# Performance work log

Hardware: AMD Instinct MI355X
Metric: run time of the kernel (lower is better)

Reference implementation:

```python
import jax, jax.numpy as jnp
import numpy as np

B, C, H, W, HEADS = 4, 192, 128, 128, 8
C2 = 2 * C
DN = ('NCHW', 'OIHW', 'NCHW')


def conv1x1(x, w, b):
    o = jax.lax.conv_general_dilated(x, w, (1, 1), 'VALID', dimension_numbers=DN)
    return o + b[None, :, None, None]


def gconv3(x, w, b):
    # grouped 3x3 conv: groups = C, channels = 2C -> 2 in / 2 out channels per group
    o = jax.lax.conv_general_dilated(x, w, (1, 1), 'SAME', dimension_numbers=DN,
                                     feature_group_count=C)
    return o + b[None, :, None, None]


def l2norm(t):
    # torch F.normalize(dim=-1, eps=1e-12)
    n = jnp.linalg.norm(t, axis=-1, keepdims=True)
    return t / jnp.maximum(n, 1e-12)


def setup_inputs() -> dict:
    key = jax.random.key(0)
    ks = jax.random.split(key, 16)
    s = 0.02
    inp = {
        'x': jax.random.normal(ks[0], (B, C, H, W), jnp.float32),
        'y': jax.random.normal(ks[1], (B, C, H, W), jnp.float32),
        'kv_w': jax.random.normal(ks[2], (C2, C, 1, 1), jnp.float32) * s,
        'kv_b': jax.random.normal(ks[3], (C2,), jnp.float32) * s,
        'kv_dw_w': jax.random.normal(ks[4], (C2, 2, 3, 3), jnp.float32) * s,
        'kv_dw_b': jax.random.normal(ks[5], (C2,), jnp.float32) * s,
        'q_w': jax.random.normal(ks[6], (C2, C, 1, 1), jnp.float32) * s,
        'q_b': jax.random.normal(ks[7], (C2,), jnp.float32) * s,
        'q_dw_w': jax.random.normal(ks[8], (C2, 2, 3, 3), jnp.float32) * s,
        'q_dw_b': jax.random.normal(ks[9], (C2,), jnp.float32) * s,
        'ky_w': jax.random.normal(ks[10], (C2, C, 1, 1), jnp.float32) * s,
        'ky_b': jax.random.normal(ks[11], (C2,), jnp.float32) * s,
        'ky_dw_w': jax.random.normal(ks[12], (C2, 2, 3, 3), jnp.float32) * s,
        'ky_dw_b': jax.random.normal(ks[13], (C2,), jnp.float32) * s,
        'temperature': jnp.ones((HEADS, 1, 1), jnp.float32),
        'gamma1': jnp.full((1,), 0.1, jnp.float32),
        'gamma2': jnp.full((1,), 0.1, jnp.float32),
    }
    return inp


def reference(x, y, kv_w, kv_b, kv_dw_w, kv_dw_b, q_w, q_b, q_dw_w, q_dw_b,
              ky_w, ky_b, ky_dw_w, ky_dw_b, temperature, gamma1, gamma2):
    b, c, h, w = x.shape
    ch = c // HEADS  # channels per head

    x_mid = x + y
    q = gconv3(conv1x1(x_mid, kv_w, kv_b), kv_dw_w, kv_dw_b)
    q1, q2 = jnp.split(q, 2, axis=1)
    kvx = gconv3(conv1x1(x, q_w, q_b), q_dw_w, q_dw_b)
    kx, vx = jnp.split(kvx, 2, axis=1)
    kvy = gconv3(conv1x1(y, ky_w, ky_b), ky_dw_w, ky_dw_b)
    ky_, vy = jnp.split(kvy, 2, axis=1)

    def to_heads(t):  # (b, head*ch, h, w) -> (b, head, ch, h*w)
        return t.reshape(b, HEADS, ch, h * w)

    q1, q2, kx, ky_, vx, vy = map(to_heads, (q1, q2, kx, ky_, vx, vy))
    q1, q2, kx, ky_ = map(l2norm, (q1, q2, kx, ky_))

    attn = (jnp.einsum('bhcn,bhdn->bhcd', q1, ky_) +
            jnp.einsum('bhcn,bhdn->bhcd', q2, kx)) * temperature[None]
    attn = jax.nn.softmax(attn, axis=-1)  # (b, head, c, c), tiny c

    out1 = jnp.einsum('bhcd,bhdn->bhcn', attn, vx)
    out2 = jnp.einsum('bhcd,bhdn->bhcn', attn, vy)
    out = gamma1[0] * out1 + gamma2[0] * out2
    return out.reshape(b, c, h, w)
```

## Files before the change

kernel.cpp:

```cpp
#include <hip/hip_runtime.h>
#include <hip/hip_bf16.h>
#include <stdint.h>

#define NUM_B 4
#define NUM_C 192
#define NUM_C2 384
#define NUM_H 128
#define NUM_W 128
#define NUM_N 16384
#define NHEADS 8
#define CHD 24

#define NKC 128
#define PSTRIDE 1280
#define LROWF 132

typedef float f32x4_t __attribute__((ext_vector_type(4)));
typedef float f32x2_t __attribute__((ext_vector_type(2)));
typedef __bf16 bf16x8_t __attribute__((ext_vector_type(8)));
typedef unsigned short u16x8_t __attribute__((ext_vector_type(8)));
typedef unsigned short u16x4_t __attribute__((ext_vector_type(4)));

__device__ __forceinline__ float bf2f(unsigned short u){
  union { unsigned int i; float f; } v; v.i = ((unsigned int)u) << 16; return v.f;
}
__device__ __forceinline__ unsigned short f2bf(float f){
  union { float f; unsigned int i; } v; v.f = f;
  unsigned int x = v.i;
  x += 0x7fffu + ((x >> 16) & 1u);
  return (unsigned short)(x >> 16);
}
__device__ __forceinline__ unsigned short f2bf_n(float f){
  union { __bf16 h; unsigned short u; } cv; cv.h = (__bf16)f; return cv.u;
}

__global__ __launch_bounds__(256) void prepack_w3(
    const float* __restrict__ W0, const float* __restrict__ W1,
    const float* __restrict__ W2, unsigned short* __restrict__ out)
{
  int tid = blockIdx.x * 256 + threadIdx.x;
  if (tid >= 9216) return;
  const float* W = (blockIdx.y == 0) ? W0 : (blockIdx.y == 1) ? W1 : W2;
  unsigned short* o_ = out + (size_t)blockIdx.y * 73728;
  int c = tid & 3;
  int o = (tid >> 2) & 127;
  int s = (tid >> 9) % 6;
  int ot = tid / 3072;
  int sw = c ^ ((o >> 1) & 3);
  const float* src = W + (size_t)(ot * 128 + o) * NUM_C + s * 32 + sw * 8;
  f32x4_t f0 = *(const f32x4_t*)src;
  f32x4_t f1 = *(const f32x4_t*)(src + 4);
  u16x8_t pk;
  pk[0] = f2bf(f0[0]); pk[1] = f2bf(f0[1]); pk[2] = f2bf(f0[2]); pk[3] = f2bf(f0[3]);
  pk[4] = f2bf(f1[0]); pk[5] = f2bf(f1[1]); pk[6] = f2bf(f1[2]); pk[7] = f2bf(f1[3]);
  *(u16x8_t*)(o_ + (size_t)tid * 8) = pk;
}

__global__ __launch_bounds__(256) void prepack_in(
    const float* __restrict__ x, const float* __restrict__ y,
    unsigned short* __restrict__ xb, unsigned short* __restrict__ yb)
{
  __shared__ __align__(16) float LX[32 * LROWF];
  __shared__ __align__(16) float LY[32 * LROWF];
  const int t = threadIdx.x;
  const int nt = blockIdx.x, s = blockIdx.y, b = blockIdx.z;
  const float* px = x + (size_t)b * NUM_C * NUM_N + (size_t)s * 32 * NUM_N + nt * 128;
  const float* py = y + (size_t)b * NUM_C * NUM_N + (size_t)s * 32 * NUM_N + nt * 128;
  #pragma unroll
  for (int i = 0; i < 4; i++){
    int idx = t + 256 * i;
    int k = idx >> 5, n4 = idx & 31;
    f32x4_t vx4 = *(const f32x4_t*)(px + (size_t)k * NUM_N + n4 * 4);
    f32x4_t vy4 = *(const f32x4_t*)(py + (size_t)k * NUM_N + n4 * 4);
    int col = (n4 * 4) ^ ((k >> 3) << 3);
    *(f32x4_t*)(&LX[k * LROWF + col]) = vx4;
    *(f32x4_t*)(&LY[k * LROWF + col]) = vy4;
  }
  __syncthreads();
  size_t obase = ((size_t)(b * 128 + nt) * 6 + s) * 4096;
  #pragma unroll
  for (int i = 0; i < 2; i++){
    int u = t + 256 * i;
    int n = u >> 2, slot = u & 3;
    int c = slot ^ ((n >> 1) & 3);
    int colr = n ^ (c << 3);
    u16x8_t ox, oy;
    #pragma unroll
    for (int kk = 0; kk < 8; kk++){
      ox[kk] = f2bf_n(LX[(c * 8 + kk) * LROWF + colr]);
      oy[kk] = f2bf_n(LY[(c * 8 + kk) * LROWF + colr]);
    }
    *(u16x8_t*)(xb + obase + (size_t)u * 8) = ox;
    *(u16x8_t*)(yb + obase + (size_t)u * 8) = oy;
  }
}

__global__ __launch_bounds__(256, 4) void conv1x1_fused(
    const unsigned short* __restrict__ xb, const unsigned short* __restrict__ yb,
    const unsigned short* __restrict__ Wpk,
    const float* __restrict__ b0, const float* __restrict__ b1,
    const float* __restrict__ b2, unsigned short* __restrict__ z3)
{
  __shared__ __align__(16) unsigned short As[2][4096];
  __shared__ __align__(16) unsigned short Bs[2][4096];
  const int d = blockIdx.x;
  const int xcd = d & 7;
  const int rest = d >> 3;
  const int j = rest % 9;
  const int m_ = (rest / 9) * 8 + xcd;
  const int br = j / 3;
  const int ot = j % 3;
  const int nt = m_ & 127;
  const int b  = m_ >> 7;
  const int t = threadIdx.x;
  const int lane = t & 63;
  const int wv = t >> 6;
  const int wr = wv >> 1, wc = wv & 1;
  const int n0 = nt * 128;

  const unsigned short* Bp0 = (br == 2) ? yb : xb;
  const unsigned short* Bp1 = yb;
  const int add2 = (br == 0);
  const unsigned short* Wb = Wpk + (size_t)br * 73728;
  const float* bias = (br == 0) ? b0 : (br == 1) ? b1 : b2;
  unsigned short* zout = z3 + (size_t)br * NUM_B * NUM_C2 * NUM_N;

  f32x4_t acc[4][4];
  const f32x4_t zz = {0.f, 0.f, 0.f, 0.f};
  #pragma unroll
  for (int m = 0; m < 4; m++)
    #pragma unroll
    for (int nf = 0; nf < 4; nf++) acc[m][nf] = zz;

  u16x8_t areg[2], breg[2], breg2[2];

  auto loadA = [&](int ks){
    const u16x8_t* gp = (const u16x8_t*)(Wb + (size_t)(ot * 6 + ks) * 4096);
    areg[0] = gp[t];
    areg[1] = gp[t + 256];
  };
  auto loadB = [&](int ks){
    size_t off = ((size_t)(b * 128 + nt) * 6 + ks) * 4096;
    const u16x8_t* gp = (const u16x8_t*)(Bp0 + off);
    breg[0] = gp[t];
    breg[1] = gp[t + 256];
    if (add2){
      const u16x8_t* gp2 = (const u16x8_t*)(Bp1 + off);
      breg2[0] = gp2[t];
      breg2[1] = gp2[t + 256];
    }
  };
  auto writeA = [&](int buf){
    *(u16x8_t*)(&As[buf][(size_t)t * 8]) = areg[0];
    *(u16x8_t*)(&As[buf][(size_t)(t + 256) * 8]) = areg[1];
  };
  auto writeB = [&](int buf){
    if (!add2){
      *(u16x8_t*)(&Bs[buf][(size_t)t * 8]) = breg[0];
      *(u16x8_t*)(&Bs[buf][(size_t)(t + 256) * 8]) = breg[1];
    } else {
      #pragma unroll
      for (int i = 0; i < 2; i++){
        u16x8_t r;
        #pragma unroll
        for (int jj = 0; jj < 8; jj++)
          r[jj] = f2bf_n(bf2f(breg[i][jj]) + bf2f(breg2[i][jj]));
        *(u16x8_t*)(&Bs[buf][(size_t)(t + 256 * i) * 8]) = r;
      }
    }
  };

  auto compute = [&](int buf){
    const int rsel = lane & 15;
    const int g = lane >> 4;
    bf16x8_t af[4], bfr[4];
    #pragma unroll
    for (int m = 0; m < 4; m++){
      int r = wr * 64 + m * 16 + rsel;
      int sw = g ^ ((r >> 1) & 3);
      af[m] = *(const bf16x8_t*)(&As[buf][r * 32 + sw * 8]);
    }
    #pragma unroll
    for (int nf = 0; nf < 4; nf++){
      int r = wc * 64 + nf * 16 + rsel;
      int sw = g ^ ((r >> 1) & 3);
      bfr[nf] = *(const bf16x8_t*)(&Bs[buf][r * 32 + sw * 8]);
    }
    #pragma unroll
    for (int m = 0; m < 4; m++)
      #pragma unroll
      for (int nf = 0; nf < 4; nf++)
        acc[m][nf] = __builtin_amdgcn_mfma_f32_16x16x32_bf16(af[m], bfr[nf], acc[m][nf], 0, 0, 0);
  };

  loadA(0); loadB(0);
  writeA(0); writeB(0);
  __syncthreads();
  int buf = 0;
  #pragma unroll 1
  for (int ks = 0; ks < 6; ks++){
    if (ks < 5){
      loadA(ks + 1);
      loadB(ks + 1);
    }
    compute(buf);
    if (ks < 5){
      writeA(buf ^ 1);
      writeB(buf ^ 1);
      __syncthreads();
    }
    buf ^= 1;
  }

  const int colb = lane & 15;
  const int ob_l = lane >> 4;
  #pragma unroll
  for (int m = 0; m < 4; m++){
    int o_blk = ot * 32 + wr * 16 + m * 4 + ob_l;
    #pragma unroll
    for (int nf = 0; nf < 4; nf++){
      int col = n0 + wc * 64 + nf * 16 + colb;
      u16x4_t pk;
      #pragma unroll
      for (int r = 0; r < 4; r++)
        pk[r] = f2bf_n(acc[m][nf][r] + bias[o_blk * 4 + r]);
      *(u16x4_t*)(zout + (((size_t)b * 96 + o_blk) * NUM_N + col) * 4) = pk;
    }
  }
}

__global__ __launch_bounds__(256) void gconv4_dw(
    const unsigned short* __restrict__ zp,
    const float* __restrict__ dww, const float* __restrict__ dwb,
    unsigned short* __restrict__ outq)
{
  const int t = threadIdx.x;
  const int wo = t & 15;
  const int hh = t >> 4;
  const int h = blockIdx.x * 16 + hh;
  const int g2 = blockIdx.y;
  const int b = blockIdx.z;

  float v[4][3][8];
  const unsigned short* src = zp + (size_t)(b * 96 + g2) * NUM_N * 4;
  #pragma unroll
  for (int dy = 0; dy < 3; dy++){
    int row = h + dy - 1;
    if (row >= 0 && row < NUM_H){
      const unsigned short* base = src + (size_t)(row * NUM_W + wo * 8) * 4;
      u16x8_t ch[4];
      #pragma unroll
      for (int q = 0; q < 4; q++) ch[q] = *(const u16x8_t*)(base + q * 8);
      #pragma unroll
      for (int jw = 0; jw < 8; jw++)
        #pragma unroll
        for (int c = 0; c < 4; c++){
          int idx = jw * 4 + c;
          v[c][dy][jw] = bf2f(ch[idx >> 3][idx & 7]);
        }
    } else {
      #pragma unroll
      for (int c = 0; c < 4; c++)
        #pragma unroll
        for (int jw = 0; jw < 8; jw++) v[c][dy][jw] = 0.f;
    }
  }
  float lft[4][3], rgt[4][3];
  #pragma unroll
  for (int c = 0; c < 4; c++)
    #pragma unroll
    for (int dy = 0; dy < 3; dy++){
      float l = __shfl_up(v[c][dy][7], 1u, 64);
      float r = __shfl_down(v[c][dy][0], 1u, 64);
      lft[c][dy] = (wo == 0)  ? 0.f : l;
      rgt[c][dy] = (wo == 15) ? 0.f : r;
    }
  #pragma unroll
  for (int c = 0; c < 4; c++){
    const int oc = g2 * 4 + c;
    const int ci0 = c & 2;
    float wgt[2][9];
    #pragma unroll
    for (int icg = 0; icg < 2; icg++)
      #pragma unroll
      for (int k9 = 0; k9 < 9; k9++)
        wgt[icg][k9] = dww[(size_t)oc * 18 + icg * 9 + k9];
    float bia = dwb[oc];
    u16x8_t st;
    #pragma unroll
    for (int w8 = 0; w8 < 8; w8++){
      float s = bia;
      #pragma unroll
      for (int icg = 0; icg < 2; icg++){
        const int ci = ci0 + icg;
        #pragma unroll
        for (int ky = 0; ky < 3; ky++)
          #pragma unroll
          for (int kx = 0; kx < 3; kx++){
            int wx = w8 + kx - 1;
            float xv = (wx < 0) ? lft[ci][ky] : ((wx > 7) ? rgt[ci][ky] : v[ci][ky][wx]);
            s += wgt[icg][ky * 3 + kx] * xv;
          }
      }
      st[w8] = f2bf(s);
    }
    *(u16x8_t*)(outq + ((size_t)b * NUM_C2 + oc) * NUM_N + h * NUM_W + wo * 8) = st;
  }
}

__global__ __launch_bounds__(64) void dots_kernel(
    const unsigned short* __restrict__ qkv0, const unsigned short* __restrict__ qkv1,
    const unsigned short* __restrict__ qkv2, float* __restrict__ dpart)
{
  const int lane = threadIdx.x;
  const int kc = blockIdx.x;
  const int h = blockIdx.y;
  const int b = blockIdx.z;
  const unsigned short* q1 = qkv0 + ((size_t)b * NUM_C2 + h * CHD) * NUM_N;
  const unsigned short* q2 = qkv0 + ((size_t)b * NUM_C2 + NUM_C + h * CHD) * NUM_N;
  const unsigned short* kx = qkv1 + ((size_t)b * NUM_C2 + h * CHD) * NUM_N;
  const unsigned short* ky = qkv2 + ((size_t)b * NUM_C2 + h * CHD) * NUM_N;

  const f32x4_t zz = {0.f, 0.f, 0.f, 0.f};
  f32x4_t d1[2][2], d2[2][2], nrm[4][2];
  #pragma unroll
  for (int i = 0; i < 2; i++)
    #pragma unroll
    for (int j = 0; j < 2; j++){ d1[i][j] = zz; d2[i][j] = zz; }
  #pragma unroll
  for (int tn = 0; tn < 4; tn++){ nrm[tn][0] = zz; nrm[tn][1] = zz; }

  const int row = lane & 15;
  const int kl = (lane >> 4) * 8;
  const int r0 = row;
  const int r1 = (16 + row < CHD) ? (16 + row) : (CHD - 1);
  #pragma unroll
  for (int ks = 0; ks < 4; ks++){
    const size_t k0 = (size_t)kc * 128 + ks * 32 + kl;
    const size_t off0 = (size_t)r0 * NUM_N + k0;
    const size_t off1 = (size_t)r1 * NUM_N + k0;
    bf16x8_t fq1[2], fq2[2], fkx[2], fky[2];
    fq1[0] = *(const bf16x8_t*)(q1 + off0);  fq1[1] = *(const bf16x8_t*)(q1 + off1);
    fq2[0] = *(const bf16x8_t*)(q2 + off0);  fq2[1] = *(const bf16x8_t*)(q2 + off1);
    fkx[0] = *(const bf16x8_t*)(kx + off0);  fkx[1] = *(const bf16x8_t*)(kx + off1);
    fky[0] = *(const bf16x8_t*)(ky + off0);  fky[1] = *(const bf16x8_t*)(ky + off1);
    #pragma unroll
    for (int i = 0; i < 2; i++)
      #pragma unroll
      for (int j = 0; j < 2; j++){
        d1[i][j] = __builtin_amdgcn_mfma_f32_16x16x32_bf16(fq1[i], fky[j], d1[i][j], 0, 0, 0);
        d2[i][j] = __builtin_amdgcn_mfma_f32_16x16x32_bf16(fq2[i], fkx[j], d2[i][j], 0, 0, 0);
      }
    #pragma unroll
    for (int rg = 0; rg < 2; rg++){
      nrm[0][rg] = __builtin_amdgcn_mfma_f32_16x16x32_bf16(fq1[rg], fq1[rg], nrm[0][rg], 0, 0, 0);
      nrm[1][rg] = __builtin_amdgcn_mfma_f32_16x16x32_bf16(fq2[rg], fq2[rg], nrm[1][rg], 0, 0, 0);
      nrm[2][rg] = __builtin_amdgcn_mfma_f32_16x16x32_bf16(fkx[rg], fkx[rg], nrm[2][rg], 0, 0, 0);
      nrm[3][rg] = __builtin_amdgcn_mfma_f32_16x16x32_bf16(fky[rg], fky[rg], nrm[3][rg], 0, 0, 0);
    }
  }

  float* P = dpart + ((size_t)kc * (NUM_B * NHEADS) + (b * NHEADS + h)) * PSTRIDE;
  const int colb = lane & 15;
  const int rb = (lane >> 4) * 4;
  #pragma unroll
  for (int i = 0; i < 2; i++)
    #pragma unroll
    for (int j = 0; j < 2; j++){
      int cc = j * 16 + colb;
      if (cc < CHD){
        #pragma unroll
        for (int r = 0; r < 4; r++){
          int rr = i * 16 + rb + r;
          if (rr < CHD){
            P[rr * CHD + cc] = d1[i][j][r];
            P[576 + rr * CHD + cc] = d2[i][j][r];
          }
        }
      }
    }
  #pragma unroll
  for (int tn = 0; tn < 4; tn++)
    #pragma unroll
    for (int rg = 0; rg < 2; rg++){
      int cc = rg * 16 + colb;
      #pragma unroll
      for (int r = 0; r < 4; r++){
        int rr = rg * 16 + rb + r;
        if (rr == cc && rr < CHD) P[1152 + tn * CHD + rr] = nrm[tn][rg][r];
      }
    }
}

__global__ __launch_bounds__(256) void reduce_dots(
    const float* __restrict__ dpart,
    float* __restrict__ dots1, float* __restrict__ dots2, float* __restrict__ norms)
{
  const int slot = blockIdx.x * 256 + threadIdx.x;
  const int bh = blockIdx.y;
  if (slot >= 1248) return;
  float s = 0.f;
  #pragma unroll 4
  for (int kc = 0; kc < NKC; kc++)
    s += dpart[((size_t)kc * (NUM_B * NHEADS) + bh) * PSTRIDE + slot];
  if (slot < 576)        dots1[(size_t)bh * 576 + slot] = s;
  else if (slot < 1152)  dots2[(size_t)bh * 576 + (slot - 576)] = s;
  else                   norms[(size_t)bh * 96 + (slot - 1152)] = s;
}

__global__ __launch_bounds__(64) void softmax_kernel(
    const float* __restrict__ dots1, const float* __restrict__ dots2,
    const float* __restrict__ norms, const float* __restrict__ temp,
    float* __restrict__ attn)
{
  const int c = threadIdx.x;
  const int bh = blockIdx.x;
  if (c >= CHD) return;
  const int h = bh & 7;
  const float* D1 = dots1 + (size_t)bh * CHD * CHD;
  const float* D2 = dots2 + (size_t)bh * CHD * CHD;
  const float* NB = norms + (size_t)bh * 4 * CHD;
  float n1 = fmaxf(sqrtf(NB[0 * CHD + c]), 1e-12f);
  float n2 = fmaxf(sqrtf(NB[1 * CHD + c]), 1e-12f);
  float T = temp[h];
  float l[CHD];
  float m = -1e30f;
  #pragma unroll
  for (int d = 0; d < CHD; d++){
    float nx = fmaxf(sqrtf(NB[2 * CHD + d]), 1e-12f);
    float ny = fmaxf(sqrtf(NB[3 * CHD + d]), 1e-12f);
    float e = (D1[c * CHD + d] / (n1 * ny) + D2[c * CHD + d] / (n2 * nx)) * T;
    l[d] = e; m = fmaxf(m, e);
  }
  float s = 0.f;
  #pragma unroll
  for (int d = 0; d < CHD; d++){ float p = expf(l[d] - m); l[d] = p; s += p; }
  float inv = 1.f / s;
  float* A = attn + (size_t)bh * CHD * CHD + c * CHD;
  #pragma unroll
  for (int d = 0; d < CHD; d++) A[d] = l[d] * inv;
}

__global__ __launch_bounds__(256) void out_kernel(
    const unsigned short* __restrict__ qkv1, const unsigned short* __restrict__ qkv2,
    const float* __restrict__ attn,
    const float* __restrict__ g1, const float* __restrict__ g2,
    float* __restrict__ out)
{
  __shared__ float A[CHD * CHD];
  const int t = threadIdx.x;
  const int nc = blockIdx.x, hq = blockIdx.y, b = blockIdx.z;
  const float* Ag = attn + (size_t)(b * NHEADS + hq) * CHD * CHD;
  for (int i = t; i < CHD * CHD; i += 256) A[i] = Ag[i];
  __syncthreads();
  const int n = nc * 512 + t * 2;
  const unsigned short* vx = qkv1 + ((size_t)b * NUM_C2 + NUM_C + hq * CHD) * NUM_N + n;
  const unsigned short* vy = qkv2 + ((size_t)b * NUM_C2 + NUM_C + hq * CHD) * NUM_N + n;
  float vxa[CHD], vxb[CHD], vya[CHD], vyb[CHD];
  #pragma unroll
  for (int d = 0; d < CHD; d++){
    unsigned int rx = *(const unsigned int*)(vx + (size_t)d * NUM_N);
    unsigned int ry = *(const unsigned int*)(vy + (size_t)d * NUM_N);
    vxa[d] = bf2f((unsigned short)(rx & 0xffffu));
    vxb[d] = bf2f((unsigned short)(rx >> 16));
    vya[d] = bf2f((unsigned short)(ry & 0xffffu));
    vyb[d] = bf2f((unsigned short)(ry >> 16));
  }
  const float G1 = g1[0], G2 = g2[0];
  float* ob = out + ((size_t)b * NUM_C + hq * CHD) * NUM_N + n;
  #pragma unroll
  for (int cq = 0; cq < CHD; cq++){
    float ax = 0.f, bx = 0.f, ay = 0.f, by = 0.f;
    #pragma unroll
    for (int d = 0; d < CHD; d++){
      float a = A[cq * CHD + d];
      ax += a * vxa[d]; bx += a * vxb[d];
      ay += a * vya[d]; by += a * vyb[d];
    }
    f32x2_t st = {G1 * ax + G2 * ay, G1 * bx + G2 * by};
    *(f32x2_t*)(ob + (size_t)cq * NUM_N) = st;
  }
}

extern "C" void kernel_launch(void* const* d_in, const int* in_sizes, int n_in,
                              void* d_out, int out_size, void* d_ws, size_t ws_size,
                              hipStream_t stream)
{
  const float* x = (const float*)d_in[0];
  const float* y = (const float*)d_in[1];
  const float* conv_b[3] = {(const float*)d_in[3], (const float*)d_in[7], (const float*)d_in[11]};
  const float* dw_w[3]   = {(const float*)d_in[4], (const float*)d_in[8], (const float*)d_in[12]};
  const float* dw_b[3]   = {(const float*)d_in[5], (const float*)d_in[9], (const float*)d_in[13]};
  const float* conv_w[3] = {(const float*)d_in[2], (const float*)d_in[6], (const float*)d_in[10]};
  const float* temp = (const float*)d_in[14];
  const float* g1 = (const float*)d_in[15];
  const float* g2 = (const float*)d_in[16];
  float* out = (float*)d_out;

  char* ws = (char*)d_ws;
  const size_t ZB = (size_t)NUM_B * NUM_C2 * NUM_N * 2;
  unsigned short* xb   = (unsigned short*)ws;
  unsigned short* yb   = (unsigned short*)(ws + 25165824);
  unsigned short* z3   = (unsigned short*)(ws + 50331648);
  unsigned short* qkv0 = (unsigned short*)ws;
  unsigned short* qkv1 = (unsigned short*)(ws + 50331648);
  unsigned short* qkv2 = (unsigned short*)(ws + 100663296);
  float* dpart         = (float*)(ws + 150994944);
  float* dots1 = (float*)(ws + 201326592);
  float* dots2 = dots1 + NUM_B * NHEADS * CHD * CHD;
  float* norms = dots2 + NUM_B * NHEADS * CHD * CHD;
  float* attn  = norms + NUM_B * NHEADS * 4 * CHD;
  unsigned short* Wpk = (unsigned short*)(attn + NUM_B * NHEADS * CHD * CHD);

  prepack_w3<<<dim3(36, 3), 256, 0, stream>>>(conv_w[0], conv_w[1], conv_w[2], Wpk);
  prepack_in<<<dim3(128, 6, NUM_B), 256, 0, stream>>>(x, y, xb, yb);

  conv1x1_fused<<<4608, 256, 0, stream>>>(xb, yb, Wpk,
                                          conv_b[0], conv_b[1], conv_b[2], z3);

  dim3 gd(NUM_H / 16, 96, NUM_B), bd(256);
  unsigned short* zb0 = z3;
  unsigned short* zb1 = z3 + ZB / 2;
  unsigned short* zb2 = z3 + ZB;
  gconv4_dw<<<gd, bd, 0, stream>>>(zb0, dw_w[0], dw_b[0], qkv0);
  gconv4_dw<<<gd, bd, 0, stream>>>(zb1, dw_w[1], dw_b[1], qkv1);
  gconv4_dw<<<gd, bd, 0, stream>>>(zb2, dw_w[2], dw_b[2], qkv2);

  dots_kernel<<<dim3(NKC, NHEADS, NUM_B), 64, 0, stream>>>(qkv0, qkv1, qkv2, dpart);
  reduce_dots<<<dim3(5, NUM_B * NHEADS), 256, 0, stream>>>(dpart, dots1, dots2, norms);
  softmax_kernel<<<dim3(NUM_B * NHEADS), 64, 0, stream>>>(dots1, dots2, norms, temp, attn);
  out_kernel<<<dim3(32, NHEADS, NUM_B), 256, 0, stream>>>(qkv1, qkv2, attn, g1, g2, out);
}
```

Before: 240.5 us.

## Stage GEMM tiles via direct global-to-LDS loads and split attention reduction finer

Replaces the register round-trip for weight tiles (and for activation tiles on branches without the x+y add) with global_load_lds direct-to-LDS transfers, removing the separate LDS write pass and cutting register pressure. The x+y branch keeps the register path because it must add the two inputs before storing. The attention-logit reduction kernel is also split into twice as many chunks, each covering 64 columns instead of 128, to raise parallelism. The async loads rely on the existing __syncthreads for completion, and more chunks mean more partial results to reduce afterwards.

```diff
diff --git a/kernel.cpp b/kernel.cpp
--- a/kernel.cpp
+++ b/kernel.cpp
@@ -11,7 +11,7 @@
 #define NHEADS 8
 #define CHD 24
 
-#define NKC 128
+#define NKC 256
 #define PSTRIDE 1280
 #define LROWF 132
 
@@ -132,41 +132,43 @@
     #pragma unroll
     for (int nf = 0; nf < 4; nf++) acc[m][nf] = zz;
 
-  u16x8_t areg[2], breg[2], breg2[2];
-
-  auto loadA = [&](int ks){
-    const u16x8_t* gp = (const u16x8_t*)(Wb + (size_t)(ot * 6 + ks) * 4096);
-    areg[0] = gp[t];
-    areg[1] = gp[t + 256];
+  u16x8_t breg[2], breg2[2];
+
+  auto stageA = [&](int ks, int buf){
+    const unsigned short* gp = Wb + (size_t)(ot * 6 + ks) * 4096 + (size_t)t * 8;
+    __builtin_amdgcn_global_load_lds(
+        (const __attribute__((address_space(1))) unsigned int*)gp,
+        (__attribute__((address_space(3))) unsigned int*)&As[buf][wv * 512], 16, 0, 0);
+    __builtin_amdgcn_global_load_lds(
+        (const __attribute__((address_space(1))) unsigned int*)(gp + 2048),
+        (__attribute__((address_space(3))) unsigned int*)&As[buf][2048 + wv * 512], 16, 0, 0);
   };
-  auto loadB = [&](int ks){
+  auto stageB_async = [&](int ks, int buf){
+    const unsigned short* gp = Bp0 + ((size_t)(b * 128 + nt) * 6 + ks) * 4096 + (size_t)t * 8;
+    __builtin_amdgcn_global_load_lds(
+        (const __attribute__((address_space(1))) unsigned int*)gp,
+        (__attribute__((address_space(3))) unsigned int*)&Bs[buf][wv * 512], 16, 0, 0);
+    __builtin_amdgcn_global_load_lds(
+        (const __attribute__((address_space(1))) unsigned int*)(gp + 2048),
+        (__attribute__((address_space(3))) unsigned int*)&Bs[buf][2048 + wv * 512], 16, 0, 0);
+  };
+  auto loadB0 = [&](int ks){
     size_t off = ((size_t)(b * 128 + nt) * 6 + ks) * 4096;
     const u16x8_t* gp = (const u16x8_t*)(Bp0 + off);
     breg[0] = gp[t];
     breg[1] = gp[t + 256];
-    if (add2){
-      const u16x8_t* gp2 = (const u16x8_t*)(Bp1 + off);
-      breg2[0] = gp2[t];
-      breg2[1] = gp2[t + 256];
-    }
+    const u16x8_t* gp2 = (const u16x8_t*)(Bp1 + off);
+    breg2[0] = gp2[t];
+    breg2[1] = gp2[t + 256];
   };
-  auto writeA = [&](int buf){
-    *(u16x8_t*)(&As[buf][(size_t)t * 8]) = areg[0];
-    *(u16x8_t*)(&As[buf][(size_t)(t + 256) * 8]) = areg[1];
-  };
-  auto writeB = [&](int buf){
-    if (!add2){
-      *(u16x8_t*)(&Bs[buf][(size_t)t * 8]) = breg[0];
-      *(u16x8_t*)(&Bs[buf][(size_t)(t + 256) * 8]) = breg[1];
-    } else {
-      #pragma unroll
-      for (int i = 0; i < 2; i++){
-        u16x8_t r;
-        #pragma unroll
-        for (int jj = 0; jj < 8; jj++)
-          r[jj] = f2bf_n(bf2f(breg[i][jj]) + bf2f(breg2[i][jj]));
-        *(u16x8_t*)(&Bs[buf][(size_t)(t + 256 * i) * 8]) = r;
-      }
+  auto writeB0 = [&](int buf){
+    #pragma unroll
+    for (int i = 0; i < 2; i++){
+      u16x8_t r;
+      #pragma unroll
+      for (int jj = 0; jj < 8; jj++)
+        r[jj] = f2bf_n(bf2f(breg[i][jj]) + bf2f(breg2[i][jj]));
+      *(u16x8_t*)(&Bs[buf][(size_t)(t + 256 * i) * 8]) = r;
     }
   };
 
@@ -193,20 +195,22 @@
         acc[m][nf] = __builtin_amdgcn_mfma_f32_16x16x32_bf16(af[m], bfr[nf], acc[m][nf], 0, 0, 0);
   };
 
-  loadA(0); loadB(0);
-  writeA(0); writeB(0);
+  stageA(0, 0);
+  if (add2){ loadB0(0); writeB0(0); }
+  else stageB_async(0, 0);
   __syncthreads();
+
   int buf = 0;
   #pragma unroll 1
   for (int ks = 0; ks < 6; ks++){
     if (ks < 5){
-      loadA(ks + 1);
-      loadB(ks + 1);
+      stageA(ks + 1, buf ^ 1);
+      if (add2) loadB0(ks + 1);
+      else stageB_async(ks + 1, buf ^ 1);
     }
     compute(buf);
     if (ks < 5){
-      writeA(buf ^ 1);
-      writeB(buf ^ 1);
+      if (add2) writeB0(buf ^ 1);
       __syncthreads();
     }
     buf ^= 1;
@@ -335,8 +339,8 @@
   const int r0 = row;
   const int r1 = (16 + row < CHD) ? (16 + row) : (CHD - 1);
   #pragma unroll
-  for (int ks = 0; ks < 4; ks++){
-    const size_t k0 = (size_t)kc * 128 + ks * 32 + kl;
+  for (int ks = 0; ks < 2; ks++){
+    const size_t k0 = (size_t)kc * 64 + ks * 32 + kl;
     const size_t off0 = (size_t)r0 * NUM_N + k0;
     const size_t off1 = (size_t)r1 * NUM_N + k0;
     bf16x8_t fq1[2], fq2[2], fkx[2], fky[2];
```

Result: slower. 251.6 us (+4.6%).
